# Kernel tuning notes

Measured on AMD Instinct MI355X. Metric: run time of the kernel, lower is better.

## Reference

```python
import jax, jax.numpy as jnp
import numpy as np

N_NODES = 100000
N_EDGES = 1600000


def _leaky_relu(x, slope=0.1):
    return jnp.where(x > 0, x, slope * x)


def _sage_conv(x, src, dst, Wl, Wr, b, n_nodes):
    # mean aggregation of source messages onto target nodes (PyG SAGEConv, aggr='mean')
    msg = x[src]                                              # [E, d] gather
    agg_sum = jax.ops.segment_sum(msg, dst, num_segments=n_nodes)
    cnt = jax.ops.segment_sum(jnp.ones((src.shape[0],), x.dtype), dst, num_segments=n_nodes)
    agg = agg_sum / jnp.maximum(cnt, 1.0)[:, None]            # empty neighborhoods -> 0
    # out = lin_l(agg) + lin_r(x); bias lives in lin_l
    return agg @ Wl + x @ Wr + b


def setup_inputs() -> dict:
    key = jax.random.key(0)
    ks = jax.random.split(key, 8)
    x = jax.random.normal(ks[0], (N_NODES, 128), dtype=jnp.float32)
    edge_index = jax.random.randint(ks[1], (2, N_EDGES), 0, N_NODES, dtype=jnp.int32)
    scale = 0.05
    Wl_stack = jax.random.normal(ks[2], (3, 128, 128), dtype=jnp.float32) * scale
    Wr_stack = jax.random.normal(ks[3], (3, 128, 128), dtype=jnp.float32) * scale
    b_stack = jax.random.normal(ks[4], (3, 128), dtype=jnp.float32) * scale
    Wl_out = jax.random.normal(ks[5], (128, 64), dtype=jnp.float32) * scale
    Wr_out = jax.random.normal(ks[6], (128, 64), dtype=jnp.float32) * scale
    b_out = jax.random.normal(ks[7], (64,), dtype=jnp.float32) * scale
    return {"x": x, "edge_index": edge_index, "Wl_stack": Wl_stack,
            "Wr_stack": Wr_stack, "b_stack": b_stack,
            "Wl_out": Wl_out, "Wr_out": Wr_out, "b_out": b_out}


def reference(x, edge_index, Wl_stack, Wr_stack, b_stack, Wl_out, Wr_out, b_out):
    src, dst = edge_index[0], edge_index[1]
    n = x.shape[0]
    h = x
    # conv1 + hidden convs, each followed by LeakyReLU(0.1)
    for i in range(Wl_stack.shape[0]):
        h = _leaky_relu(_sage_conv(h, src, dst, Wl_stack[i], Wr_stack[i], b_stack[i], n))
    # final SAGEConv without activation
    out = _sage_conv(h, src, dst, Wl_out, Wr_out, b_out, n)
    return out
```

## Files before the change

kernel.cpp:

```cpp
#include <hip/hip_runtime.h>

#define NN 100000
#define NNP 100096
#define NE 1600000
#define NBK 391
#define CAP 4608
#define SCCH 4096
#define NSC ((NE + SCCH - 1) / SCCH)
#define MMG 782

typedef __attribute__((ext_vector_type(8))) short bf16x8;
typedef __attribute__((ext_vector_type(4))) float f32x4;

__device__ __forceinline__ float bf2f(unsigned short u) {
    unsigned int v = ((unsigned int)u) << 16;
    return __builtin_bit_cast(float, v);
}
__device__ __forceinline__ unsigned short f2bf(float f) {
    unsigned int u = __builtin_bit_cast(unsigned int, f);
    u += 0x7FFFu + ((u >> 16) & 1u);
    return (unsigned short)(u >> 16);
}
__device__ __forceinline__ unsigned int pk2(float lo, float hi) {
    return (unsigned int)f2bf(lo) | ((unsigned int)f2bf(hi) << 16);
}
__device__ __forceinline__ float bflo(unsigned int v) {
    return __builtin_bit_cast(float, v << 16);
}
__device__ __forceinline__ float bfhi(unsigned int v) {
    return __builtin_bit_cast(float, v & 0xFFFF0000u);
}

__device__ __forceinline__ int mm_gmap(int bid, int off) {
    int x = (bid + off) & 7;
    int j = bid >> 3;
    int g = j;
#pragma unroll
    for (int u = 0; u < 8; ++u)
        if (u < x) g += ((((u - off) & 7) < 6) ? 98 : 97);
    return g;
}


__global__ __launch_bounds__(256) void k_prep(const float* __restrict__ Wl_stack,
                                              const float* __restrict__ Wr_stack,
                                              const float* __restrict__ Wl_out,
                                              const float* __restrict__ Wr_out,
                                              unsigned short* __restrict__ WT,
                                              int* __restrict__ bcur) {
    int i = blockIdx.x * 256 + threadIdx.x;
    const int L3OFF = 3 * 256 * 128;
    const int TOT = L3OFF + 128 * 128;
    if (i < TOT) {
        float v;
        if (i < L3OFF) {
            int l = i / (256 * 128);
            int r = i % (256 * 128);
            int c = r / 128;
            int k = r % 128;
            v = (c < 128) ? Wl_stack[(size_t)(l * 128 + k) * 128 + c]
                          : Wr_stack[(size_t)(l * 128 + k) * 128 + (c - 128)];
        } else {
            int r = i - L3OFF;
            int c = r / 128;
            int k = r % 128;
            v = (c < 64) ? Wl_out[(size_t)k * 64 + c]
                         : Wr_out[(size_t)k * 64 + (c - 64)];
        }
        WT[i] = f2bf(v);
    } else if (i - TOT < NBK) {
        bcur[i - TOT] = (i - TOT) * CAP;
    }
}


__global__ __launch_bounds__(256) void k_scatter(const int* __restrict__ src,
                                                 const int* __restrict__ dst,
                                                 int* __restrict__ bcur,
                                                 unsigned int* __restrict__ ebuf) {
    __shared__ int lh[NBK], lbase[NBK];
    int tid = threadIdx.x;
    for (int i = tid; i < NBK; i += 256) lh[i] = 0;
    __syncthreads();
    int base = blockIdx.x * SCCH;
    int lim = min(SCCH, NE - base);
    for (int i = tid; i < lim; i += 256)
        atomicAdd(&lh[dst[base + i] >> 8], 1);
    __syncthreads();
    for (int i = tid; i < NBK; i += 256)
        lbase[i] = lh[i] ? atomicAdd(&bcur[i], lh[i]) : 0;
    __syncthreads();
    for (int i = tid; i < NBK; i += 256) lh[i] = 0;
    __syncthreads();
    for (int i = tid; i < lim; i += 256) {
        int d = dst[base + i];
        int s = src[base + i];
        int b = d >> 8;
        int off = atomicAdd(&lh[b], 1);
        ebuf[(size_t)lbase[b] + off] = ((unsigned)s << 8) | (unsigned)(d & 255);
    }
}


template <int NOUT, bool F32IN>
__device__ __forceinline__ void mm_body(int bid, int xoff, int tid,
                                        const void* __restrict__ Ain,
                                        const unsigned short* __restrict__ WT,
                                        unsigned short* __restrict__ Y,
                                        unsigned short* __restrict__ Z,
                                        unsigned char* lds) {
    constexpr int HALVES = NOUT / 64;
    int wave = tid >> 6, l = tid & 63;
    int lrow = l & 15, g = l >> 4;
    int half, rowblk;
    if (HALVES == 2) {
        int gm = mm_gmap(bid, xoff);
        half = gm & 1;
        rowblk = gm >> 1;
    } else {
        half = 0;
        rowblk = bid;
    }
    int rbase = rowblk * 256 + wave * 64;

    {
        const unsigned char* wsrc = (const unsigned char*)(WT + (size_t)half * 128 * 128);
#pragma unroll
        for (int j = 0; j < 8; ++j) {
            int lin = (j * 256 + tid) * 16;
            uint4 v = *(const uint4*)(wsrc + lin);
            int row = lin >> 8;
            int colb = lin & 255;
            *(uint4*)(lds + row * 256 + (colb ^ ((row & 7) << 4))) = v;
        }
    }

    bf16x8 af[4][4];
#pragma unroll
    for (int s = 0; s < 4; ++s) {
        int row = rbase + s * 16 + lrow;
#pragma unroll
        for (int ks = 0; ks < 4; ++ks) {
            if (F32IN) {
                int rc = row < NN ? row : NN - 1;
                const float* ap = (const float*)Ain + (size_t)rc * 128 + ks * 32 + g * 8;
                float4 a = *(const float4*)ap;
                float4 b = *(const float4*)(ap + 4);
                uint4 u;
                u.x = pk2(a.x, a.y); u.y = pk2(a.z, a.w);
                u.z = pk2(b.x, b.y); u.w = pk2(b.z, b.w);
                af[s][ks] = __builtin_bit_cast(bf16x8, u);
            } else {
                af[s][ks] = *(const bf16x8*)((const unsigned short*)Ain
                                             + (size_t)row * 128 + ks * 32 + g * 8);
            }
        }
    }
    __syncthreads();

#pragma unroll
    for (int cg = 0; cg < 8; ++cg) {
        int c0 = cg * 16;
        int rl = c0 + lrow;
        bf16x8 bfr[4];
#pragma unroll
        for (int ks = 0; ks < 4; ++ks) {
            int colb = ks * 64 + g * 16;
            bfr[ks] = *(const bf16x8*)(lds + rl * 256 + (colb ^ ((rl & 7) << 4)));
        }
        int gc0 = half * 128 + c0;
        unsigned short* dstp = (gc0 < NOUT) ? Y : Z;
        int cb = ((gc0 < NOUT) ? gc0 : gc0 - NOUT) + g * 4;
#pragma unroll
        for (int s = 0; s < 4; ++s) {
            f32x4 acc = {0.f, 0.f, 0.f, 0.f};
#pragma unroll
            for (int ks = 0; ks < 4; ++ks)
                acc = __builtin_amdgcn_mfma_f32_16x16x32_bf16(bfr[ks], af[s][ks], acc, 0, 0, 0);
            int row = rbase + s * 16 + lrow;
            uint2 w;
            w.x = pk2(acc[0], acc[1]);
            w.y = pk2(acc[2], acc[3]);
            *(uint2*)(dstp + (size_t)row * NOUT + cb) = w;
        }
    }
}

__device__ __forceinline__ void csr_body(int bkt, int tid,
                                         const unsigned int* __restrict__ ebuf,
                                         const int* __restrict__ bcur,
                                         int* __restrict__ row_beg,
                                         int* __restrict__ row_end,
                                         int* __restrict__ csr,
                                         unsigned char* smem) {
    int* sdeg = (int*)smem;
    int* spre = sdeg + 256;
    int nbase = bkt << 8;
    int ebeg = bkt * CAP;
    int eend = bcur[bkt];
    sdeg[tid] = 0;
    __syncthreads();
    for (int e = ebeg + tid; e < eend; e += 256)
        atomicAdd(&sdeg[ebuf[e] & 255], 1);
    __syncthreads();
    spre[tid] = sdeg[tid];
    __syncthreads();
#pragma unroll
    for (int off = 1; off < 256; off <<= 1) {
        int t = (tid >= off) ? spre[tid - off] : 0;
        __syncthreads();
        if (tid >= off) spre[tid] += t;
        __syncthreads();
    }
    int excl = spre[tid] - sdeg[tid];
    if (nbase + tid < NN) {
        row_beg[nbase + tid] = ebeg + excl;
        row_end[nbase + tid] = ebeg + excl + sdeg[tid];
    }
    __syncthreads();
    sdeg[tid] = excl;
    __syncthreads();
    for (int e = ebeg + tid; e < eend; e += 256) {
        unsigned int v = ebuf[e];
        int p = atomicAdd(&sdeg[v & 255], 1);
        csr[ebeg + p] = (int)(v >> 8);
    }
}


__global__ __launch_bounds__(256) void k_fused1(const unsigned int* __restrict__ ebuf,
                                                const int* __restrict__ bcur,
                                                int* __restrict__ row_beg,
                                                int* __restrict__ row_end,
                                                int* __restrict__ csr,
                                                const float* __restrict__ x,
                                                const unsigned short* __restrict__ WT,
                                                unsigned short* __restrict__ Y,
                                                unsigned short* __restrict__ Z) {
    __shared__ unsigned char smem[32768];
    int tid = threadIdx.x;
    if (blockIdx.x < NBK) {
        csr_body(blockIdx.x, tid, ebuf, bcur, row_beg, row_end, csr, smem);
    } else {
        mm_body<128, true>(blockIdx.x - NBK, 7, tid, x, WT, Y, Z, smem);
    }
}


template <int NOUT>
__global__ __launch_bounds__(256) void k_mm(const unsigned short* __restrict__ Ain,
                                            const unsigned short* __restrict__ WT,
                                            unsigned short* __restrict__ Y,
                                            unsigned short* __restrict__ Z) {
    __shared__ unsigned char lds[32768];
    mm_body<NOUT, false>(blockIdx.x, 0, threadIdx.x, Ain, WT, Y, Z, lds);
}


template <int NOUT, bool RELU>
__global__ __launch_bounds__(256) void k_aggb(const unsigned short* __restrict__ Y,
                                              const unsigned short* __restrict__ Z,
                                              const int* __restrict__ row_beg,
                                              const int* __restrict__ row_end,
                                              const int* __restrict__ csr,
                                              const float* __restrict__ b,
                                              unsigned short* __restrict__ outb,
                                              float* __restrict__ outf) {
    int lane = threadIdx.x & 63;
    int n = __builtin_amdgcn_readfirstlane(blockIdx.x * 4 + (threadIdx.x >> 6));
    if (n >= NN) return;
    int beg = __builtin_amdgcn_readfirstlane(row_beg[n]);
    int end = __builtin_amdgcn_readfirstlane(row_end[n]);
    float inv = (end > beg) ? 1.0f / (float)(end - beg) : 0.0f;

    if (NOUT == 128) {
        const int lane2 = lane * 2;
        float a0 = 0.f, a1 = 0.f;
        int e = beg;
        for (; e + 8 <= end; e += 8) {
            int s0 = csr[e + 0], s1 = csr[e + 1], s2 = csr[e + 2], s3 = csr[e + 3];
            int s4 = csr[e + 4], s5 = csr[e + 5], s6 = csr[e + 6], s7 = csr[e + 7];
            unsigned int v0 = *(const unsigned int*)(Y + (size_t)s0 * 128 + lane2);
            unsigned int v1 = *(const unsigned int*)(Y + (size_t)s1 * 128 + lane2);
            unsigned int v2 = *(const unsigned int*)(Y + (size_t)s2 * 128 + lane2);
            unsigned int v3 = *(const unsigned int*)(Y + (size_t)s3 * 128 + lane2);
            unsigned int v4 = *(const unsigned int*)(Y + (size_t)s4 * 128 + lane2);
            unsigned int v5 = *(const unsigned int*)(Y + (size_t)s5 * 128 + lane2);
            unsigned int v6 = *(const unsigned int*)(Y + (size_t)s6 * 128 + lane2);
            unsigned int v7 = *(const unsigned int*)(Y + (size_t)s7 * 128 + lane2);
            a0 += bflo(v0) + bflo(v1) + bflo(v2) + bflo(v3)
                + bflo(v4) + bflo(v5) + bflo(v6) + bflo(v7);
            a1 += bfhi(v0) + bfhi(v1) + bfhi(v2) + bfhi(v3)
                + bfhi(v4) + bfhi(v5) + bfhi(v6) + bfhi(v7);
        }
        for (; e + 4 <= end; e += 4) {
            int s0 = csr[e + 0], s1 = csr[e + 1], s2 = csr[e + 2], s3 = csr[e + 3];
            unsigned int v0 = *(const unsigned int*)(Y + (size_t)s0 * 128 + lane2);
            unsigned int v1 = *(const unsigned int*)(Y + (size_t)s1 * 128 + lane2);
            unsigned int v2 = *(const unsigned int*)(Y + (size_t)s2 * 128 + lane2);
            unsigned int v3 = *(const unsigned int*)(Y + (size_t)s3 * 128 + lane2);
            a0 += bflo(v0) + bflo(v1) + bflo(v2) + bflo(v3);
            a1 += bfhi(v0) + bfhi(v1) + bfhi(v2) + bfhi(v3);
        }
        for (; e < end; ++e) {
            int s = csr[e];
            unsigned int v = *(const unsigned int*)(Y + (size_t)s * 128 + lane2);
            a0 += bflo(v);
            a1 += bfhi(v);
        }
        unsigned int zv = *(const unsigned int*)(Z + (size_t)n * 128 + lane2);
        float2 bb = *(const float2*)(b + lane2);
        float o0 = a0 * inv + bflo(zv) + bb.x;
        float o1 = a1 * inv + bfhi(zv) + bb.y;
        if (RELU) {
            o0 = o0 > 0.f ? o0 : 0.1f * o0;
            o1 = o1 > 0.f ? o1 : 0.1f * o1;
        }
        *(unsigned int*)(outb + (size_t)n * 128 + lane2) = pk2(o0, o1);
    } else {
        float a0 = 0.f;
        int e = beg;
        for (; e + 8 <= end; e += 8) {
            int s0 = csr[e + 0], s1 = csr[e + 1], s2 = csr[e + 2], s3 = csr[e + 3];
            int s4 = csr[e + 4], s5 = csr[e + 5], s6 = csr[e + 6], s7 = csr[e + 7];
            float f0 = bf2f(Y[(size_t)s0 * 64 + lane]);
            float f1 = bf2f(Y[(size_t)s1 * 64 + lane]);
            float f2 = bf2f(Y[(size_t)s2 * 64 + lane]);
            float f3 = bf2f(Y[(size_t)s3 * 64 + lane]);
            float f4 = bf2f(Y[(size_t)s4 * 64 + lane]);
            float f5 = bf2f(Y[(size_t)s5 * 64 + lane]);
            float f6 = bf2f(Y[(size_t)s6 * 64 + lane]);
            float f7 = bf2f(Y[(size_t)s7 * 64 + lane]);
            a0 += f0 + f1 + f2 + f3 + f4 + f5 + f6 + f7;
        }
        for (; e + 4 <= end; e += 4) {
            int s0 = csr[e + 0], s1 = csr[e + 1], s2 = csr[e + 2], s3 = csr[e + 3];
            float f0 = bf2f(Y[(size_t)s0 * 64 + lane]);
            float f1 = bf2f(Y[(size_t)s1 * 64 + lane]);
            float f2 = bf2f(Y[(size_t)s2 * 64 + lane]);
            float f3 = bf2f(Y[(size_t)s3 * 64 + lane]);
            a0 += f0 + f1 + f2 + f3;
        }
        for (; e < end; ++e) {
            int s = csr[e];
            a0 += bf2f(Y[(size_t)s * 64 + lane]);
        }
        float o = a0 * inv + bf2f(Z[(size_t)n * 64 + lane]) + b[lane];
        if (RELU) o = o > 0.f ? o : 0.1f * o;
        outf[(size_t)n * 64 + lane] = o;
    }
}


extern "C" void kernel_launch(void* const* d_in, const int* in_sizes, int n_in,
                              void* d_out, int out_size, void* d_ws, size_t ws_size,
                              hipStream_t stream) {
    const float* x        = (const float*)d_in[0];
    const int*   ei       = (const int*)d_in[1];
    const float* Wl_stack = (const float*)d_in[2];
    const float* Wr_stack = (const float*)d_in[3];
    const float* b_stack  = (const float*)d_in[4];
    const float* Wl_out   = (const float*)d_in[5];
    const float* Wr_out   = (const float*)d_in[6];
    const float* b_out    = (const float*)d_in[7];
    float* out = (float*)d_out;

    unsigned short* hb = (unsigned short*)d_ws;
    unsigned short* Yb = hb + (size_t)NNP * 128;
    unsigned short* Zb = Yb + (size_t)NNP * 128;
    unsigned short* WT = Zb + (size_t)NNP * 128;
    unsigned int* ebuf = (unsigned int*)(WT + 114688);
    int* csr     = (int*)(ebuf + (size_t)NBK * CAP);
    int* row_beg = csr + (size_t)NBK * CAP;
    int* row_end = row_beg + NN;
    int* bcur    = row_end + NN;

    const int* src = ei;
    const int* dst = ei + NE;

    k_prep<<<450, 256, 0, stream>>>(Wl_stack, Wr_stack, Wl_out, Wr_out, WT, bcur);

    k_scatter<<<NSC, 256, 0, stream>>>(src, dst, bcur, ebuf);

    k_fused1<<<NBK + MMG, 256, 0, stream>>>(ebuf, bcur, row_beg, row_end, csr,
                                            x, WT, Yb, Zb);

    k_aggb<128, true><<<(NN + 3) / 4, 256, 0, stream>>>(Yb, Zb, row_beg, row_end, csr,
                                                        b_stack, hb, nullptr);
    for (int l = 1; l < 3; ++l) {
        k_mm<128><<<MMG, 256, 0, stream>>>(hb, WT + l * 32768, Yb, Zb);
        k_aggb<128, true><<<(NN + 3) / 4, 256, 0, stream>>>(Yb, Zb, row_beg, row_end, csr,
                                                            b_stack + l * 128, hb, nullptr);
    }
    k_mm<64><<<NNP / 256, 256, 0, stream>>>(hb, WT + 98304, Yb, Zb);
    k_aggb<64, false><<<(NN + 3) / 4, 256, 0, stream>>>(Yb, Zb, row_beg, row_end, csr,
                                                        b_out, nullptr, out);
}
```

Measured before the change: 357.3 us.

## Merge weight prep into scatter kernel and halve rows per block in final matmul

The separate weight-transpose kernel is folded into the edge-scatter kernel as extra blocks, which now use 512 threads. The bucket-cursor initialisation moves to a hipMemsetAsync, so bcur holds relative counts and the scatter and CSR code add the bucket base. The final 64-wide matmul now processes 128 rows per block instead of 256, launching twice as many blocks. The aim is to remove a launch and improve parallelism in the last matmul, at the cost of a memset call and reloading the weight tile into LDS in more blocks.

```diff
diff --git a/kernel.cpp b/kernel.cpp
--- a/kernel.cpp
+++ b/kernel.cpp
@@ -8,6 +8,7 @@
 #define SCCH 4096
 #define NSC ((NE + SCCH - 1) / SCCH)
 #define MMG 782
+#define PREPB 224
 
 typedef __attribute__((ext_vector_type(8))) short bf16x8;
 typedef __attribute__((ext_vector_type(4))) float f32x4;
@@ -42,57 +43,54 @@
 }
 
 
-__global__ __launch_bounds__(256) void k_prep(const float* __restrict__ Wl_stack,
-                                              const float* __restrict__ Wr_stack,
-                                              const float* __restrict__ Wl_out,
-                                              const float* __restrict__ Wr_out,
-                                              unsigned short* __restrict__ WT,
-                                              int* __restrict__ bcur) {
-    int i = blockIdx.x * 256 + threadIdx.x;
-    const int L3OFF = 3 * 256 * 128;
-    const int TOT = L3OFF + 128 * 128;
-    if (i < TOT) {
-        float v;
-        if (i < L3OFF) {
-            int l = i / (256 * 128);
-            int r = i % (256 * 128);
-            int c = r / 128;
-            int k = r % 128;
-            v = (c < 128) ? Wl_stack[(size_t)(l * 128 + k) * 128 + c]
-                          : Wr_stack[(size_t)(l * 128 + k) * 128 + (c - 128)];
-        } else {
-            int r = i - L3OFF;
-            int c = r / 128;
-            int k = r % 128;
-            v = (c < 64) ? Wl_out[(size_t)k * 64 + c]
-                         : Wr_out[(size_t)k * 64 + (c - 64)];
-        }
-        WT[i] = f2bf(v);
-    } else if (i - TOT < NBK) {
-        bcur[i - TOT] = (i - TOT) * CAP;
-    }
-}
-
-
-__global__ __launch_bounds__(256) void k_scatter(const int* __restrict__ src,
-                                                 const int* __restrict__ dst,
-                                                 int* __restrict__ bcur,
-                                                 unsigned int* __restrict__ ebuf) {
+__global__ __launch_bounds__(512) void k_sp(const int* __restrict__ src,
+                                            const int* __restrict__ dst,
+                                            int* __restrict__ bcur,
+                                            unsigned int* __restrict__ ebuf,
+                                            const float* __restrict__ Wl_stack,
+                                            const float* __restrict__ Wr_stack,
+                                            const float* __restrict__ Wl_out,
+                                            const float* __restrict__ Wr_out,
+                                            unsigned short* __restrict__ WT) {
+    int tid = threadIdx.x;
+    if (blockIdx.x >= NSC) {
+        int i = (blockIdx.x - NSC) * 512 + tid;
+        const int L3OFF = 3 * 256 * 128;
+        const int TOT = L3OFF + 128 * 128;
+        if (i < TOT) {
+            float v;
+            if (i < L3OFF) {
+                int l = i / (256 * 128);
+                int r = i % (256 * 128);
+                int c = r / 128;
+                int k = r % 128;
+                v = (c < 128) ? Wl_stack[(size_t)(l * 128 + k) * 128 + c]
+                              : Wr_stack[(size_t)(l * 128 + k) * 128 + (c - 128)];
+            } else {
+                int r = i - L3OFF;
+                int c = r / 128;
+                int k = r % 128;
+                v = (c < 64) ? Wl_out[(size_t)k * 64 + c]
+                             : Wr_out[(size_t)k * 64 + (c - 64)];
+            }
+            WT[i] = f2bf(v);
+        }
+        return;
+    }
     __shared__ int lh[NBK], lbase[NBK];
-    int tid = threadIdx.x;
-    for (int i = tid; i < NBK; i += 256) lh[i] = 0;
+    for (int i = tid; i < NBK; i += 512) lh[i] = 0;
     __syncthreads();
     int base = blockIdx.x * SCCH;
     int lim = min(SCCH, NE - base);
-    for (int i = tid; i < lim; i += 256)
+    for (int i = tid; i < lim; i += 512)
         atomicAdd(&lh[dst[base + i] >> 8], 1);
     __syncthreads();
-    for (int i = tid; i < NBK; i += 256)
-        lbase[i] = lh[i] ? atomicAdd(&bcur[i], lh[i]) : 0;
-    __syncthreads();
-    for (int i = tid; i < NBK; i += 256) lh[i] = 0;
-    __syncthreads();
-    for (int i = tid; i < lim; i += 256) {
+    for (int i = tid; i < NBK; i += 512)
+        lbase[i] = lh[i] ? (i * CAP + atomicAdd(&bcur[i], lh[i])) : 0;
+    __syncthreads();
+    for (int i = tid; i < NBK; i += 512) lh[i] = 0;
+    __syncthreads();
+    for (int i = tid; i < lim; i += 512) {
         int d = dst[base + i];
         int s = src[base + i];
         int b = d >> 8;
@@ -102,7 +100,7 @@
 }
 
 
-template <int NOUT, bool F32IN>
+template <int NOUT, bool F32IN, int S>
 __device__ __forceinline__ void mm_body(int bid, int xoff, int tid,
                                         const void* __restrict__ Ain,
                                         const unsigned short* __restrict__ WT,
@@ -121,7 +119,7 @@
         half = 0;
         rowblk = bid;
     }
-    int rbase = rowblk * 256 + wave * 64;
+    int rbase = rowblk * (S * 64) + wave * (S * 16);
 
     {
         const unsigned char* wsrc = (const unsigned char*)(WT + (size_t)half * 128 * 128);
@@ -135,9 +133,9 @@
         }
     }
 
-    bf16x8 af[4][4];
-#pragma unroll
-    for (int s = 0; s < 4; ++s) {
+    bf16x8 af[S][4];
+#pragma unroll
+    for (int s = 0; s < S; ++s) {
         int row = rbase + s * 16 + lrow;
 #pragma unroll
         for (int ks = 0; ks < 4; ++ks) {
@@ -172,7 +170,7 @@
         unsigned short* dstp = (gc0 < NOUT) ? Y : Z;
         int cb = ((gc0 < NOUT) ? gc0 : gc0 - NOUT) + g * 4;
 #pragma unroll
-        for (int s = 0; s < 4; ++s) {
+        for (int s = 0; s < S; ++s) {
             f32x4 acc = {0.f, 0.f, 0.f, 0.f};
 #pragma unroll
             for (int ks = 0; ks < 4; ++ks)
@@ -197,7 +195,7 @@
     int* spre = sdeg + 256;
     int nbase = bkt << 8;
     int ebeg = bkt * CAP;
-    int eend = bcur[bkt];
+    int eend = ebeg + bcur[bkt];
     sdeg[tid] = 0;
     __syncthreads();
     for (int e = ebeg + tid; e < eend; e += 256)
@@ -242,18 +240,18 @@
     if (blockIdx.x < NBK) {
         csr_body(blockIdx.x, tid, ebuf, bcur, row_beg, row_end, csr, smem);
     } else {
-        mm_body<128, true>(blockIdx.x - NBK, 7, tid, x, WT, Y, Z, smem);
-    }
-}
-
-
-template <int NOUT>
+        mm_body<128, true, 4>(blockIdx.x - NBK, 7, tid, x, WT, Y, Z, smem);
+    }
+}
+
+
+template <int NOUT, int S>
 __global__ __launch_bounds__(256) void k_mm(const unsigned short* __restrict__ Ain,
                                             const unsigned short* __restrict__ WT,
                                             unsigned short* __restrict__ Y,
                                             unsigned short* __restrict__ Z) {
     __shared__ unsigned char lds[32768];
-    mm_body<NOUT, false>(blockIdx.x, 0, threadIdx.x, Ain, WT, Y, Z, lds);
+    mm_body<NOUT, false, S>(blockIdx.x, 0, threadIdx.x, Ain, WT, Y, Z, lds);
 }
 
 
@@ -378,9 +376,10 @@
     const int* src = ei;
     const int* dst = ei + NE;
 
-    k_prep<<<450, 256, 0, stream>>>(Wl_stack, Wr_stack, Wl_out, Wr_out, WT, bcur);
-
-    k_scatter<<<NSC, 256, 0, stream>>>(src, dst, bcur, ebuf);
+    (void)hipMemsetAsync(bcur, 0, NBK * sizeof(int), stream);
+
+    k_sp<<<NSC + PREPB, 512, 0, stream>>>(src, dst, bcur, ebuf,
+                                          Wl_stack, Wr_stack, Wl_out, Wr_out, WT);
 
     k_fused1<<<NBK + MMG, 256, 0, stream>>>(ebuf, bcur, row_beg, row_end, csr,
                                             x, WT, Yb, Zb);
@@ -388,11 +387,11 @@
     k_aggb<128, true><<<(NN + 3) / 4, 256, 0, stream>>>(Yb, Zb, row_beg, row_end, csr,
                                                         b_stack, hb, nullptr);
     for (int l = 1; l < 3; ++l) {
-        k_mm<128><<<MMG, 256, 0, stream>>>(hb, WT + l * 32768, Yb, Zb);
+        k_mm<128, 4><<<MMG, 256, 0, stream>>>(hb, WT + l * 32768, Yb, Zb);
         k_aggb<128, true><<<(NN + 3) / 4, 256, 0, stream>>>(Yb, Zb, row_beg, row_end, csr,
                                                             b_stack + l * 128, hb, nullptr);
     }
-    k_mm<64><<<NNP / 256, 256, 0, stream>>>(hb, WT + 98304, Yb, Zb);
+    k_mm<64, 2><<<NNP / 128, 256, 0, stream>>>(hb, WT + 98304, Yb, Zb);
     k_aggb<64, false><<<(NN + 3) / 4, 256, 0, stream>>>(Yb, Zb, row_beg, row_end, csr,
                                                         b_out, nullptr, out);
 }
```

After: 356.8 us. About the same (-0.1%).
